# Optimization experiments

Measured on AMD Instinct MI355X. Metric: run time of the kernel, lower is better.

## Reference

```python
import jax, jax.numpy as jnp
import numpy as np

B, C, H, W = 4, 256, 64, 64
HALF = C // 2
BN_EPS = 1e-5


def setup_inputs() -> dict:
    key = jax.random.key(0)
    ks = jax.random.split(key, 6)
    scale = 1.0 / np.sqrt(C)
    return {
        "x": jax.random.normal(ks[0], (B, C, H, W), dtype=jnp.float32),
        "w1": jax.random.normal(ks[1], (HALF, C), dtype=jnp.float32) * scale,
        "w2": jax.random.normal(ks[2], (HALF, C), dtype=jnp.float32) * scale,
        "w3": jax.random.normal(ks[3], (HALF, C), dtype=jnp.float32) * scale,
        "w4": jax.random.normal(ks[4], (C, HALF), dtype=jnp.float32) * (1.0 / np.sqrt(HALF)),
        "gamma": jnp.ones((C,), dtype=jnp.float32),
        "beta": jnp.zeros((C,), dtype=jnp.float32),
        "running_mean": jnp.zeros((C,), dtype=jnp.float32),
        "running_var": jnp.ones((C,), dtype=jnp.float32),
    }


def _conv1x1(x, w):
    # x: [b,c,h,w], w: [out,in] -> [b,out,h,w]
    return jnp.einsum('bchw,oc->bohw', x, w)


def reference(x, w1, w2, w3, w4, gamma, beta, running_mean, running_var):
    b, Cin, h, w = x.shape
    c = Cin // 2
    hw = h * w
    n1 = _conv1x1(x, w1)  # [b,c,h,w]
    n2 = _conv1x1(x, w2)
    n3 = _conv1x1(x, w3)
    # Faithful to torch .view (raw reshape, NOT a transpose)
    q = n1.reshape(b, hw, c)   # [b,hw,c]
    k = n2.reshape(b, c, hw)   # [b,c,hw]
    attn = jnp.einsum('bic,bcj->bij', q, k)        # [b,hw,hw]
    attn = jax.nn.softmax(attn, axis=-1)
    v = n3.reshape(b, hw, c)
    res = jnp.einsum('bij,bjc->bic', attn, v)      # [b,hw,c]
    res = res.reshape(b, c, h, w)
    out = _conv1x1(res, w4)                        # [b,C,h,w]
    # BatchNorm2d in eval mode with running stats
    inv = jax.lax.rsqrt(running_var + BN_EPS)
    out = (out - running_mean[None, :, None, None]) * (gamma * inv)[None, :, None, None] + beta[None, :, None, None]
    return out + x
```

## Files before the change

### kernel.cpp

```cpp
#include <hip/hip_runtime.h>
#include <cstdint>

#define BN 4
#define CIN 256
#define HALFC 128
#define HW 4096
#define SPLIT 4
#define JT 64
#define JITERS (HW / SPLIT / JT)

typedef float  floatx4 __attribute__((ext_vector_type(4)));
typedef short  shortx8 __attribute__((ext_vector_type(8)));

#if __has_builtin(__builtin_amdgcn_exp2f)
#define EXP2F(x) __builtin_amdgcn_exp2f(x)
#else
#define EXP2F(x) exp2f(x)
#endif
#define L2E 1.44269504088896f

__device__ __forceinline__ unsigned short f2bf(float f) {
  unsigned u = __float_as_uint(f);
  u += 0x7FFFu + ((u >> 16) & 1u);
  return (unsigned short)(u >> 16);
}
__device__ __forceinline__ float bf2f(unsigned short h) {
  return __uint_as_float((unsigned)h << 16);
}

__device__ __forceinline__ void async16(const void* g, void* l) {
  __builtin_amdgcn_global_load_lds((const __attribute__((address_space(1))) void*)g,
                                   (__attribute__((address_space(3))) void*)l, 16, 0, 0);
}

__global__ __launch_bounds__(256) void k_split(const float* __restrict__ x,
    const float* __restrict__ w1, const float* __restrict__ w2,
    const float* __restrict__ w3, unsigned short* __restrict__ Xth,
    unsigned short* __restrict__ Xtl, unsigned short* __restrict__ Wh,
    unsigned short* __restrict__ Wl) {
  __shared__ float smf[64 * 65];
  int bid = blockIdx.x;
  int t = threadIdx.x;
  if (bid < 1024) {
    int b = bid >> 8, rem = bid & 255;
    int cit = rem >> 6, pxt = rem & 63;
    const float* src = x + (size_t)b * 1048576 + (size_t)(cit * 64) * HW + pxt * 64;
#pragma unroll
    for (int k = 0; k < 16; k++) {
      int idx = k * 256 + t;
      int r = idx >> 6, c = idx & 63;
      smf[r * 65 + c] = src[(size_t)r * HW + c];
    }
    __syncthreads();
    int prow = t >> 2, seg = t & 3;
    union { unsigned short us[16]; uint4 v[2]; } oh, ol;
#pragma unroll
    for (int u = 0; u < 16; u++) {
      float v = smf[(seg * 16 + u) * 65 + prow];
      unsigned short hh = f2bf(v);
      oh.us[u] = hh;
      ol.us[u] = f2bf(v - bf2f(hh));
    }
    size_t dst = (size_t)b * 1048576 + (size_t)(pxt * 64 + prow) * 256 + cit * 64 + seg * 16;
    *(uint4*)(Xth + dst) = oh.v[0];
    *(uint4*)(Xth + dst + 8) = oh.v[1];
    *(uint4*)(Xtl + dst) = ol.v[0];
    *(uint4*)(Xtl + dst + 8) = ol.v[1];
  } else {
    int bw = bid - 1024;
    int f0 = bw * 8192 + t * 32;
    const float* wsrc;
    int fo;
    if (f0 < 32768)      { wsrc = w1; fo = f0; }
    else if (f0 < 65536) { wsrc = w2; fo = f0 - 32768; }
    else                 { wsrc = w3; fo = f0 - 65536; }
    union { unsigned short us[32]; uint4 v[4]; } oh, ol;
#pragma unroll
    for (int u = 0; u < 32; u++) {
      float v = wsrc[fo + u];
      unsigned short hh = f2bf(v);
      oh.us[u] = hh;
      ol.us[u] = f2bf(v - bf2f(hh));
    }
#pragma unroll
    for (int k = 0; k < 4; k++) {
      *((uint4*)(Wh + f0) + k) = oh.v[k];
      *((uint4*)(Wl + f0) + k) = ol.v[k];
    }
  }
}

__global__ __launch_bounds__(256) void k_projM(const unsigned short* __restrict__ Xth,
    const unsigned short* __restrict__ Xtl, const unsigned short* __restrict__ Wh,
    const unsigned short* __restrict__ Wl, unsigned short* __restrict__ Q,
    unsigned short* __restrict__ Kt, unsigned short* __restrict__ n3) {
  __shared__ unsigned short XhS[4096];
  __shared__ unsigned short XlS[4096];
  __shared__ unsigned short ES[9216];
  int bid = blockIdx.x;
  int pxt = bid & 31;
  int ct = bid >> 5;
  int b = ct / 6, cot = ct % 6;
  int px0 = pxt * 128, co0 = cot * 64;
  int t = threadIdx.x;
  int w = t >> 6, lane = t & 63, l16 = lane & 15, quad = lane >> 4;

  int myco = co0 + w * 16 + l16;
  shortx8 whf[8], wlf[8];
#pragma unroll
  for (int s = 0; s < 8; s++) {
    whf[s] = *(const shortx8*)(Wh + (size_t)myco * 256 + s * 32 + quad * 8);
    wlf[s] = *(const shortx8*)(Wl + (size_t)myco * 256 + s * 32 + quad * 8);
  }
  floatx4 acc[8];
  floatx4 zf = {0.f, 0.f, 0.f, 0.f};
#pragma unroll
  for (int mt = 0; mt < 8; mt++) acc[mt] = zf;
  const unsigned short* XhB = Xth + (size_t)b * 1048576;
  const unsigned short* XlB = Xtl + (size_t)b * 1048576;
  int k8 = lane >> 4, pxm = lane & 15;

#pragma unroll
  for (int s = 0; s < 8; s++) {
    __syncthreads();
#pragma unroll
    for (int c2 = 0; c2 < 2; c2++) {
      int px = px0 + (c2 * 4 + w) * 16 + pxm;
      size_t so = (size_t)px * 256 + s * 32 + k8 * 8;
      async16(XhB + so, (char*)XhS + c2 * 4096 + w * 1024);
      async16(XlB + so, (char*)XlS + c2 * 4096 + w * 1024);
    }
    __syncthreads();
#pragma unroll
    for (int mt = 0; mt < 8; mt++) {
      shortx8 ah = *(const shortx8*)((const char*)XhS + mt * 1024 + lane * 16);
      shortx8 al = *(const shortx8*)((const char*)XlS + mt * 1024 + lane * 16);
      acc[mt] = __builtin_amdgcn_mfma_f32_16x16x32_bf16(ah, whf[s], acc[mt], 0, 0, 0);
      acc[mt] = __builtin_amdgcn_mfma_f32_16x16x32_bf16(al, whf[s], acc[mt], 0, 0, 0);
      acc[mt] = __builtin_amdgcn_mfma_f32_16x16x32_bf16(ah, wlf[s], acc[mt], 0, 0, 0);
    }
  }
  __syncthreads();
  if (cot < 2 || cot >= 4) {
    int co_l = w * 16 + l16;
#pragma unroll
    for (int mt = 0; mt < 8; mt++) {
      int px = mt * 16 + quad * 4;
      unsigned lo = (unsigned)f2bf(acc[mt][0]) | ((unsigned)f2bf(acc[mt][1]) << 16);
      unsigned hi = (unsigned)f2bf(acc[mt][2]) | ((unsigned)f2bf(acc[mt][3]) << 16);
      *(uint2*)(ES + co_l * 136 + px) = make_uint2(lo, hi);
    }
    __syncthreads();
    int cr = t >> 2, seg = t & 3;
    unsigned short* dstb = (cot < 2)
        ? Q  + (size_t)b * 524288 + (size_t)(co0 + cr) * HW
        : n3 + (size_t)b * 524288 + (size_t)(co0 - 256 + cr) * HW;
#pragma unroll
    for (int k2 = 0; k2 < 4; k2++) {
      uint4 v = *(const uint4*)(ES + cr * 136 + seg * 32 + k2 * 8);
      *(uint4*)(dstb + px0 + seg * 32 + k2 * 8) = v;
    }
  } else {
#pragma unroll
    for (int mt = 0; mt < 8; mt++)
#pragma unroll
      for (int rr = 0; rr < 4; rr++) {
        int px = mt * 16 + quad * 4 + rr;
        ES[px * 72 + w * 16 + l16] = f2bf(acc[mt][rr]);
      }
    __syncthreads();
    int ch0 = co0 - 128;
#pragma unroll
    for (int it = 0; it < 4; it++) {
      int cid = it * 256 + t;
      int px = cid >> 3, c8 = cid & 7;
      uint4 v = *(const uint4*)(ES + px * 72 + c8 * 8);
      *(uint4*)(Kt + (size_t)b * 524288 + (size_t)(px0 + px) * 128 + ch0 + c8 * 8) = v;
    }
  }
}

__global__ __launch_bounds__(256) void k_layoutV(const unsigned short* __restrict__ n3,
    unsigned short* __restrict__ Vt) {
  __shared__ unsigned short sm[8192];
  int bid = blockIdx.x;
  int t = threadIdx.x;
  int b = bid >> 6;
  int chg = bid & 63;
  const unsigned short* src = n3 + (size_t)b * 524288 + (size_t)(chg * 2) * HW;
#pragma unroll
  for (int k = 0; k < 32; k++) {
    int idx = k * 256 + t;
    sm[idx] = src[idx];
  }
  __syncthreads();
  int c = t >> 1, half = t & 1;
  union { unsigned short us[32]; uint4 v[4]; } o;
#pragma unroll
  for (int u = 0; u < 32; u++) o.us[u] = sm[half * 4096 + u * 128 + c];
  unsigned short* d = Vt + ((size_t)b * 128 + c) * HW + chg * 64 + half * 32;
#pragma unroll
  for (int k = 0; k < 4; k++) *((uint4*)d + k) = o.v[k];
}

__global__ __launch_bounds__(256, 4) void k_flash(const unsigned short* __restrict__ Q,
    const unsigned short* __restrict__ Kt, const unsigned short* __restrict__ Vt,
    float* __restrict__ Opart, float* __restrict__ ml) {
  __shared__ unsigned short KtS[64 * 128];
  __shared__ unsigned short VtS[128 * 64];
  __shared__ unsigned short PS[4 * 16 * 64];
  int bid = blockIdx.x;
  int itile = bid & 63, sp = (bid >> 6) & 3, b = bid >> 8;
  int t = threadIdx.x;
  int w = t >> 6, lane = t & 63, l16 = lane & 15, quad = lane >> 4;
  int i0 = itile * 64;

  shortx8 qf[4];
  {
    const unsigned short* qp = Q + ((size_t)b * HW + i0 + w * 16 + l16) * 128 + quad * 8;
#pragma unroll
    for (int ks = 0; ks < 4; ks++) qf[ks] = *(const shortx8*)(qp + ks * 32);
  }
  floatx4 O[8];
  floatx4 zf = {0.f, 0.f, 0.f, 0.f};
#pragma unroll
  for (int nt = 0; nt < 8; nt++) O[nt] = zf;
  float m_i = -1e30f, l_i = 0.f;
  const unsigned short* KtB = Kt + (size_t)b * HW * 128;
  const unsigned short* VtB = Vt + (size_t)b * 128 * HW;
  char* Pw = (char*)PS + w * 2048;

  for (int it = 0; it < JITERS; it++) {
    int j0 = sp * (HW / SPLIT) + it * JT;
    __syncthreads();
#pragma unroll
    for (int c4 = 0; c4 < 4; c4++) {
      int jm = lane & 15, cc = w * 4 + (lane >> 4);
      async16(KtB + (size_t)(j0 + c4 * 16 + jm) * 128 + cc * 8,
              (char*)KtS + c4 * 4096 + w * 1024);
    }
#pragma unroll
    for (int c4 = 0; c4 < 4; c4++) {
      int cm = lane & 15, cc = (w & 1) * 4 + (lane >> 4);
      int c = (c4 * 2 + (w >> 1)) * 16 + cm;
      async16(VtB + (size_t)c * HW + j0 + cc * 8,
              (char*)VtS + c4 * 4096 + w * 1024);
    }
    __syncthreads();

    floatx4 S[4];
#pragma unroll
    for (int mt = 0; mt < 4; mt++) S[mt] = zf;
#pragma unroll
    for (int mt = 0; mt < 4; mt++) {
#pragma unroll
      for (int ks = 0; ks < 4; ks++) {
        shortx8 af = *(const shortx8*)((const char*)KtS + mt * 4096 + ks * 1024 + lane * 16);
        S[mt] = __builtin_amdgcn_mfma_f32_16x16x32_bf16(af, qf[ks], S[mt], 0, 0, 0);
      }
    }
    float tmax = S[0][0];
#pragma unroll
    for (int mt = 0; mt < 4; mt++)
#pragma unroll
      for (int rr = 0; rr < 4; rr++) tmax = fmaxf(tmax, S[mt][rr]);
    tmax = fmaxf(tmax, __shfl_xor(tmax, 16));
    tmax = fmaxf(tmax, __shfl_xor(tmax, 32));
    float mnew = fmaxf(m_i, tmax);
    float alpha = EXP2F((m_i - mnew) * L2E);
    float tsum = 0.f;
    float P[4][4];
#pragma unroll
    for (int mt = 0; mt < 4; mt++)
#pragma unroll
      for (int rr = 0; rr < 4; rr++) {
        float p = EXP2F((S[mt][rr] - mnew) * L2E);
        P[mt][rr] = p;
        tsum += p;
      }
    tsum += __shfl_xor(tsum, 16);
    tsum += __shfl_xor(tsum, 32);
    l_i = l_i * alpha + tsum;
    m_i = mnew;
    float ar[4];
#pragma unroll
    for (int rr = 0; rr < 4; rr++) ar[rr] = __shfl(alpha, quad * 4 + rr);
#pragma unroll
    for (int nt = 0; nt < 8; nt++)
#pragma unroll
      for (int rr = 0; rr < 4; rr++) O[nt][rr] *= ar[rr];
#pragma unroll
    for (int mt = 0; mt < 4; mt++) {
      unsigned lo = (unsigned)f2bf(P[mt][0]) | ((unsigned)f2bf(P[mt][1]) << 16);
      unsigned hi = (unsigned)f2bf(P[mt][2]) | ((unsigned)f2bf(P[mt][3]) << 16);
      int cc = mt * 2 + (quad >> 1);
      *(uint2*)(Pw + cc * 256 + l16 * 16 + (quad & 1) * 8) = make_uint2(lo, hi);
    }
    __threadfence_block();
#pragma unroll
    for (int kt = 0; kt < 2; kt++) {
      shortx8 pf = *(const shortx8*)(Pw + kt * 1024 + lane * 16);
#pragma unroll
      for (int nt = 0; nt < 8; nt++) {
        shortx8 vf = *(const shortx8*)((const char*)VtS + nt * 2048 + kt * 1024 + lane * 16);
        O[nt] = __builtin_amdgcn_mfma_f32_16x16x32_bf16(pf, vf, O[nt], 0, 0, 0);
      }
    }
  }
  float* Ob = Opart + ((size_t)(sp * 4 + b) * HW + i0 + w * 16) * 128;
#pragma unroll
  for (int nt = 0; nt < 8; nt++)
#pragma unroll
    for (int rr = 0; rr < 4; rr++)
      Ob[(size_t)(quad * 4 + rr) * 128 + nt * 16 + l16] = O[nt][rr];
  if (quad == 0) {
    float2* mlp = (float2*)ml;
    mlp[(size_t)(sp * 4 + b) * HW + i0 + w * 16 + l16] = make_float2(m_i, l_i);
  }
}

__global__ __launch_bounds__(256) void k_merge(const float* __restrict__ Opart,
    const float* __restrict__ ml, float* __restrict__ res) {
  size_t e = (size_t)blockIdx.x * 256 + threadIdx.x;
  int cq = (int)(e & 31);
  int i = (int)((e >> 5) & 4095);
  int b = (int)(e >> 17);
  const float2* mlp = (const float2*)ml;
  float m[SPLIT], l[SPLIT];
  float M = -1e30f;
#pragma unroll
  for (int s = 0; s < SPLIT; s++) {
    float2 st = mlp[(size_t)(s * 4 + b) * HW + i];
    m[s] = st.x; l[s] = st.y;
    M = fmaxf(M, m[s]);
  }
  float denom = 0.f;
  float wgt[SPLIT];
#pragma unroll
  for (int s = 0; s < SPLIT; s++) {
    float ws_ = EXP2F((m[s] - M) * L2E);
    wgt[s] = ws_;
    denom += l[s] * ws_;
  }
  float inv = 1.f / denom;
  floatx4 acc = {0.f, 0.f, 0.f, 0.f};
#pragma unroll
  for (int s = 0; s < SPLIT; s++) {
    floatx4 v = *(const floatx4*)(Opart + ((size_t)(s * 4 + b) * HW + i) * 128 + cq * 4);
    acc += v * (wgt[s] * inv);
  }
  *(floatx4*)(res + e * 4) = acc;
}

__global__ __launch_bounds__(256) void k_out(const float* __restrict__ res,
    const float* __restrict__ w4, const float* __restrict__ gamma,
    const float* __restrict__ beta, const float* __restrict__ rmean,
    const float* __restrict__ rvar, const float* __restrict__ x,
    float* __restrict__ out) {
  __shared__ float wt[16 * 128];
  int bid = blockIdx.x;
  int cot = bid & 15;
  int st = (bid >> 4) & 15;
  int b = bid >> 8;
  int t = threadIdx.x;
  int co0 = cot * 16;
#pragma unroll
  for (int k = 0; k < 8; k++) wt[k * 256 + t] = w4[(size_t)co0 * 128 + k * 256 + t];
  __syncthreads();
  int px = st * 256 + t;
  const float* rb = res + (size_t)b * 524288 + px;
  float acc[16];
#pragma unroll
  for (int r = 0; r < 16; r++) acc[r] = 0.f;
  for (int ci = 0; ci < 128; ci += 4) {
    float xv[4];
#pragma unroll
    for (int kk = 0; kk < 4; kk++) xv[kk] = rb[(size_t)(ci + kk) * HW];
#pragma unroll
    for (int r = 0; r < 16; r++) {
      floatx4 wv = *(const floatx4*)&wt[r * 128 + ci];
#pragma unroll
      for (int kk = 0; kk < 4; kk++) acc[r] += wv[kk] * xv[kk];
    }
  }
  const float* xb = x + ((size_t)b * 256 + co0) * HW + px;
  float* ob = out + ((size_t)b * 256 + co0) * HW + px;
#pragma unroll
  for (int r = 0; r < 16; r++) {
    int co = co0 + r;
    float g = gamma[co] * rsqrtf(rvar[co] + 1e-5f);
    float bb = beta[co] - rmean[co] * g;
    ob[(size_t)r * HW] = acc[r] * g + bb + xb[(size_t)r * HW];
  }
}

extern "C" void kernel_launch(void* const* d_in, const int* in_sizes, int n_in,
                              void* d_out, int out_size, void* d_ws, size_t ws_size,
                              hipStream_t stream) {
  const float* x     = (const float*)d_in[0];
  const float* w1    = (const float*)d_in[1];
  const float* w2    = (const float*)d_in[2];
  const float* w3    = (const float*)d_in[3];
  const float* w4    = (const float*)d_in[4];
  const float* gamma = (const float*)d_in[5];
  const float* beta  = (const float*)d_in[6];
  const float* rmean = (const float*)d_in[7];
  const float* rvar  = (const float*)d_in[8];
  float* out = (float*)d_out;
  char* ws = (char*)d_ws;

  size_t off = (size_t)SPLIT * 4 * HW * 128 * 4;
  float* Opart = (float*)ws;
  unsigned short* n3  = (unsigned short*)ws;
  unsigned short* Xth = (unsigned short*)(ws + ((size_t)8  << 20));
  unsigned short* Xtl = (unsigned short*)(ws + ((size_t)17 << 20));
  unsigned short* Q  = (unsigned short*)(ws + off); off += (size_t)4 * HW * 128 * 2;
  unsigned short* Kt = (unsigned short*)(ws + off); off += (size_t)4 * HW * 128 * 2;
  unsigned short* Vt = (unsigned short*)(ws + off); off += (size_t)4 * HW * 128 * 2;
  float* ml  = (float*)(ws + off); off += (size_t)SPLIT * 4 * HW * 2 * 4;
  float* res = (float*)(ws + off); off += (size_t)4 * HW * 128 * 4;
  unsigned short* Wh = (unsigned short*)(ws + off); off += (size_t)384 * 256 * 2;
  unsigned short* Wl = (unsigned short*)(ws + off); off += (size_t)384 * 256 * 2;
  if (ws_size < off) return;

  k_split  <<<1036, 256, 0, stream>>>(x, w1, w2, w3, Xth, Xtl, Wh, Wl);
  k_projM  <<<768,  256, 0, stream>>>(Xth, Xtl, Wh, Wl, Q, Kt, n3);
  k_layoutV<<<256,  256, 0, stream>>>(n3, Vt);
  k_flash  <<<1024, 256, 0, stream>>>(Q, Kt, Vt, Opart, ml);
  k_merge  <<<2048, 256, 0, stream>>>(Opart, ml, res);
  k_out    <<<1024, 256, 0, stream>>>(res, w4, gamma, beta, rmean, rvar, x, out);
}
```

Measured before the change: 224.6 us.

## Double query rows per warp in flash kernel to reuse K/V tiles

Each wave now handles two 16-row query groups (128 query rows per block instead of 64), so every K and V tile loaded into shared memory and every LDS fragment read feeds twice as many MFMAs. The grid halves to 512 blocks and launch bounds drop to 2 blocks per CU to make room for the doubled accumulator and score registers. The goal is less global and LDS traffic per unit of compute. The cost is fewer resident waves and fewer blocks, which gives less latency hiding and parallelism on a GPU with many CUs.

```diff
diff --git a/kernel.cpp b/kernel.cpp
--- a/kernel.cpp
+++ b/kernel.cpp
@@ -203,119 +203,138 @@
   for (int k = 0; k < 4; k++) *((uint4*)d + k) = o.v[k];
 }
 
-__global__ __launch_bounds__(256, 4) void k_flash(const unsigned short* __restrict__ Q,
+__global__ __launch_bounds__(256, 2) void k_flash(const unsigned short* __restrict__ Q,
     const unsigned short* __restrict__ Kt, const unsigned short* __restrict__ Vt,
     float* __restrict__ Opart, float* __restrict__ ml) {
   __shared__ unsigned short KtS[64 * 128];
   __shared__ unsigned short VtS[128 * 64];
-  __shared__ unsigned short PS[4 * 16 * 64];
+  __shared__ unsigned short PS[4 * 32 * 64];
   int bid = blockIdx.x;
-  int itile = bid & 63, sp = (bid >> 6) & 3, b = bid >> 8;
+  int itile = bid & 31, sp = (bid >> 5) & 3, b = bid >> 7;
   int t = threadIdx.x;
   int w = t >> 6, lane = t & 63, l16 = lane & 15, quad = lane >> 4;
-  int i0 = itile * 64;
-
-  shortx8 qf[4];
-  {
-    const unsigned short* qp = Q + ((size_t)b * HW + i0 + w * 16 + l16) * 128 + quad * 8;
-#pragma unroll
-    for (int ks = 0; ks < 4; ks++) qf[ks] = *(const shortx8*)(qp + ks * 32);
-  }
-  floatx4 O[8];
+  int i0 = itile * 128;
+
+  shortx8 qf[2][4];
+#pragma unroll
+  for (int ig = 0; ig < 2; ig++) {
+    const unsigned short* qp = Q + ((size_t)b * HW + i0 + w * 32 + ig * 16 + l16) * 128 + quad * 8;
+#pragma unroll
+    for (int ks = 0; ks < 4; ks++) qf[ig][ks] = *(const shortx8*)(qp + ks * 32);
+  }
+  floatx4 O[2][8];
   floatx4 zf = {0.f, 0.f, 0.f, 0.f};
 #pragma unroll
-  for (int nt = 0; nt < 8; nt++) O[nt] = zf;
-  float m_i = -1e30f, l_i = 0.f;
-  const unsigned short* KtB = Kt + (size_t)b * HW * 128;
-  const unsigned short* VtB = Vt + (size_t)b * 128 * HW;
-  char* Pw = (char*)PS + w * 2048;
+  for (int ig = 0; ig < 2; ig++)
+#pragma unroll
+    for (int nt = 0; nt < 8; nt++) O[ig][nt] = zf;
+  float m_i[2] = {-1e30f, -1e30f}, l_i[2] = {0.f, 0.f};
+
+  int ccK = w * 4 + (lane >> 4);
+  const unsigned short* kbase = Kt + (size_t)b * HW * 128
+                              + (size_t)(sp * 1024 + l16) * 128 + ccK * 8;
+  int ccV = (w & 1) * 4 + (lane >> 4);
+  const unsigned short* vbase = Vt + ((size_t)b * 128 + (w >> 1) * 16 + l16) * HW
+                              + sp * 1024 + ccV * 8;
+  char* Pw = (char*)PS + w * 4096;
 
   for (int it = 0; it < JITERS; it++) {
-    int j0 = sp * (HW / SPLIT) + it * JT;
-    __syncthreads();
-#pragma unroll
-    for (int c4 = 0; c4 < 4; c4++) {
-      int jm = lane & 15, cc = w * 4 + (lane >> 4);
-      async16(KtB + (size_t)(j0 + c4 * 16 + jm) * 128 + cc * 8,
-              (char*)KtS + c4 * 4096 + w * 1024);
-    }
-#pragma unroll
-    for (int c4 = 0; c4 < 4; c4++) {
-      int cm = lane & 15, cc = (w & 1) * 4 + (lane >> 4);
-      int c = (c4 * 2 + (w >> 1)) * 16 + cm;
-      async16(VtB + (size_t)c * HW + j0 + cc * 8,
-              (char*)VtS + c4 * 4096 + w * 1024);
-    }
-    __syncthreads();
-
-    floatx4 S[4];
-#pragma unroll
-    for (int mt = 0; mt < 4; mt++) S[mt] = zf;
+    __syncthreads();
+#pragma unroll
+    for (int c4 = 0; c4 < 4; c4++)
+      async16(kbase + (size_t)it * 8192 + c4 * 2048, (char*)KtS + c4 * 4096 + w * 1024);
+#pragma unroll
+    for (int c4 = 0; c4 < 4; c4++)
+      async16(vbase + (size_t)c4 * 32 * HW + it * 64, (char*)VtS + c4 * 4096 + w * 1024);
+    __syncthreads();
+
+    floatx4 S[2][4];
+#pragma unroll
+    for (int ig = 0; ig < 2; ig++)
+#pragma unroll
+      for (int mt = 0; mt < 4; mt++) S[ig][mt] = zf;
 #pragma unroll
     for (int mt = 0; mt < 4; mt++) {
 #pragma unroll
       for (int ks = 0; ks < 4; ks++) {
         shortx8 af = *(const shortx8*)((const char*)KtS + mt * 4096 + ks * 1024 + lane * 16);
-        S[mt] = __builtin_amdgcn_mfma_f32_16x16x32_bf16(af, qf[ks], S[mt], 0, 0, 0);
+        S[0][mt] = __builtin_amdgcn_mfma_f32_16x16x32_bf16(af, qf[0][ks], S[0][mt], 0, 0, 0);
+        S[1][mt] = __builtin_amdgcn_mfma_f32_16x16x32_bf16(af, qf[1][ks], S[1][mt], 0, 0, 0);
       }
     }
-    float tmax = S[0][0];
-#pragma unroll
-    for (int mt = 0; mt < 4; mt++)
-#pragma unroll
-      for (int rr = 0; rr < 4; rr++) tmax = fmaxf(tmax, S[mt][rr]);
-    tmax = fmaxf(tmax, __shfl_xor(tmax, 16));
-    tmax = fmaxf(tmax, __shfl_xor(tmax, 32));
-    float mnew = fmaxf(m_i, tmax);
-    float alpha = EXP2F((m_i - mnew) * L2E);
-    float tsum = 0.f;
-    float P[4][4];
-#pragma unroll
-    for (int mt = 0; mt < 4; mt++)
-#pragma unroll
-      for (int rr = 0; rr < 4; rr++) {
-        float p = EXP2F((S[mt][rr] - mnew) * L2E);
-        P[mt][rr] = p;
-        tsum += p;
+    float alpha[2];
+#pragma unroll
+    for (int ig = 0; ig < 2; ig++) {
+      float tmax = S[ig][0][0];
+#pragma unroll
+      for (int mt = 0; mt < 4; mt++)
+#pragma unroll
+        for (int rr = 0; rr < 4; rr++) tmax = fmaxf(tmax, S[ig][mt][rr]);
+      tmax = fmaxf(tmax, __shfl_xor(tmax, 16));
+      tmax = fmaxf(tmax, __shfl_xor(tmax, 32));
+      float mnew = fmaxf(m_i[ig], tmax);
+      alpha[ig] = EXP2F((m_i[ig] - mnew) * L2E);
+      float tsum = 0.f;
+#pragma unroll
+      for (int mt = 0; mt < 4; mt++)
+#pragma unroll
+        for (int rr = 0; rr < 4; rr++) {
+          float p = EXP2F((S[ig][mt][rr] - mnew) * L2E);
+          S[ig][mt][rr] = p;
+          tsum += p;
+        }
+      tsum += __shfl_xor(tsum, 16);
+      tsum += __shfl_xor(tsum, 32);
+      l_i[ig] = l_i[ig] * alpha[ig] + tsum;
+      m_i[ig] = mnew;
+    }
+#pragma unroll
+    for (int ig = 0; ig < 2; ig++) {
+      float ar[4];
+#pragma unroll
+      for (int rr = 0; rr < 4; rr++) ar[rr] = __shfl(alpha[ig], quad * 4 + rr);
+#pragma unroll
+      for (int nt = 0; nt < 8; nt++)
+#pragma unroll
+        for (int rr = 0; rr < 4; rr++) O[ig][nt][rr] *= ar[rr];
+    }
+#pragma unroll
+    for (int ig = 0; ig < 2; ig++)
+#pragma unroll
+      for (int mt = 0; mt < 4; mt++) {
+        unsigned lo = (unsigned)f2bf(S[ig][mt][0]) | ((unsigned)f2bf(S[ig][mt][1]) << 16);
+        unsigned hi = (unsigned)f2bf(S[ig][mt][2]) | ((unsigned)f2bf(S[ig][mt][3]) << 16);
+        *(uint2*)(Pw + ig * 2048 + (mt * 2 + (quad >> 1)) * 256 + l16 * 16 + (quad & 1) * 8)
+            = make_uint2(lo, hi);
       }
-    tsum += __shfl_xor(tsum, 16);
-    tsum += __shfl_xor(tsum, 32);
-    l_i = l_i * alpha + tsum;
-    m_i = mnew;
-    float ar[4];
-#pragma unroll
-    for (int rr = 0; rr < 4; rr++) ar[rr] = __shfl(alpha, quad * 4 + rr);
-#pragma unroll
-    for (int nt = 0; nt < 8; nt++)
-#pragma unroll
-      for (int rr = 0; rr < 4; rr++) O[nt][rr] *= ar[rr];
-#pragma unroll
-    for (int mt = 0; mt < 4; mt++) {
-      unsigned lo = (unsigned)f2bf(P[mt][0]) | ((unsigned)f2bf(P[mt][1]) << 16);
-      unsigned hi = (unsigned)f2bf(P[mt][2]) | ((unsigned)f2bf(P[mt][3]) << 16);
-      int cc = mt * 2 + (quad >> 1);
-      *(uint2*)(Pw + cc * 256 + l16 * 16 + (quad & 1) * 8) = make_uint2(lo, hi);
-    }
     __threadfence_block();
 #pragma unroll
     for (int kt = 0; kt < 2; kt++) {
-      shortx8 pf = *(const shortx8*)(Pw + kt * 1024 + lane * 16);
+      shortx8 pf0 = *(const shortx8*)(Pw + kt * 1024 + lane * 16);
+      shortx8 pf1 = *(const shortx8*)(Pw + 2048 + kt * 1024 + lane * 16);
 #pragma unroll
       for (int nt = 0; nt < 8; nt++) {
         shortx8 vf = *(const shortx8*)((const char*)VtS + nt * 2048 + kt * 1024 + lane * 16);
-        O[nt] = __builtin_amdgcn_mfma_f32_16x16x32_bf16(pf, vf, O[nt], 0, 0, 0);
+        O[0][nt] = __builtin_amdgcn_mfma_f32_16x16x32_bf16(pf0, vf, O[0][nt], 0, 0, 0);
+        O[1][nt] = __builtin_amdgcn_mfma_f32_16x16x32_bf16(pf1, vf, O[1][nt], 0, 0, 0);
       }
     }
   }
-  float* Ob = Opart + ((size_t)(sp * 4 + b) * HW + i0 + w * 16) * 128;
-#pragma unroll
-  for (int nt = 0; nt < 8; nt++)
-#pragma unroll
-    for (int rr = 0; rr < 4; rr++)
-      Ob[(size_t)(quad * 4 + rr) * 128 + nt * 16 + l16] = O[nt][rr];
+#pragma unroll
+  for (int ig = 0; ig < 2; ig++) {
+    float* Ob = Opart + ((size_t)(sp * 4 + b) * HW + i0 + w * 32 + ig * 16) * 128;
+#pragma unroll
+    for (int nt = 0; nt < 8; nt++)
+#pragma unroll
+      for (int rr = 0; rr < 4; rr++)
+        Ob[(size_t)(quad * 4 + rr) * 128 + nt * 16 + l16] = O[ig][nt][rr];
+  }
   if (quad == 0) {
     float2* mlp = (float2*)ml;
-    mlp[(size_t)(sp * 4 + b) * HW + i0 + w * 16 + l16] = make_float2(m_i, l_i);
+#pragma unroll
+    for (int ig = 0; ig < 2; ig++)
+      mlp[(size_t)(sp * 4 + b) * HW + i0 + w * 32 + ig * 16 + l16]
+          = make_float2(m_i[ig], l_i[ig]);
   }
 }
 
@@ -426,7 +445,7 @@
   k_split  <<<1036, 256, 0, stream>>>(x, w1, w2, w3, Xth, Xtl, Wh, Wl);
   k_projM  <<<768,  256, 0, stream>>>(Xth, Xtl, Wh, Wl, Q, Kt, n3);
   k_layoutV<<<256,  256, 0, stream>>>(n3, Vt);
-  k_flash  <<<1024, 256, 0, stream>>>(Q, Kt, Vt, Opart, ml);
+  k_flash  <<<512,  256, 0, stream>>>(Q, Kt, Vt, Opart, ml);
   k_merge  <<<2048, 256, 0, stream>>>(Opart, ml, res);
   k_out    <<<1024, 256, 0, stream>>>(res, w4, gamma, beta, rmean, rvar, x, out);
 }
```

New measurement: 210.9 us. -6.1%, faster.
